# Kernel optimization log

Hardware: AMD Instinct MI355X
Metric: run time of the kernel (lower is better)

## Reference

```python
import jax, jax.numpy as jnp
import numpy as np

V, D, S, L, H, NC = 32000, 768, 1024, 4, 12, 16
HS = D // H
B = 8

def _layernorm(x, w, b, eps=1e-5):
    mu = jnp.mean(x, axis=-1, keepdims=True)
    var = jnp.mean(jnp.square(x - mu), axis=-1, keepdims=True)
    return (x - mu) * jax.lax.rsqrt(var + eps) * w + b


def setup_inputs() -> dict:
    key = jax.random.key(0)
    ks = jax.random.split(key, 24)
    s = 0.02
    inp = {
        "x": jax.random.randint(ks[0], (B, S), 0, V, dtype=jnp.int64) if jax.config.jax_enable_x64 else jax.random.randint(ks[0], (B, S), 0, V, dtype=jnp.int32),
        "attention_mask": jnp.ones((B, S), dtype=jnp.int32),
        "tok_emb": jax.random.normal(ks[1], (V, D), jnp.float32) * s,
        "pos_emb": jax.random.normal(ks[2], (S, D), jnp.float32) * s,
        "Wq": jax.random.normal(ks[3], (L, H, D, HS), jnp.float32) * s,
        "Wk": jax.random.normal(ks[4], (L, H, D, HS), jnp.float32) * s,
        "Wv": jax.random.normal(ks[5], (L, H, D, HS), jnp.float32) * s,
        "Wo": jax.random.normal(ks[6], (L, D, D), jnp.float32) * s,
        "bo": jnp.zeros((L, D), jnp.float32),
        "ln1_w": jnp.ones((L, D), jnp.float32),
        "ln1_b": jnp.zeros((L, D), jnp.float32),
        "ln2_w": jnp.ones((L, D), jnp.float32),
        "ln2_b": jnp.zeros((L, D), jnp.float32),
        "W1": jax.random.normal(ks[7], (L, D, 4 * D), jnp.float32) * s,
        "b1": jnp.zeros((L, 4 * D), jnp.float32),
        "W2": jax.random.normal(ks[8], (L, 4 * D, D), jnp.float32) * s,
        "b2": jnp.zeros((L, D), jnp.float32),
        "lnf_w": jnp.ones((D,), jnp.float32),
        "lnf_b": jnp.zeros((D,), jnp.float32),
        "cW1": jax.random.normal(ks[9], (D, 4 * D), jnp.float32) * s,
        "cb1": jnp.zeros((4 * D,), jnp.float32),
        "cW2": jax.random.normal(ks[10], (4 * D, NC), jnp.float32) * s,
        "cb2": jnp.zeros((NC,), jnp.float32),
    }
    return inp


def reference(x, attention_mask, tok_emb, pos_emb, Wq, Wk, Wv, Wo, bo,
              ln1_w, ln1_b, ln2_w, ln2_b, W1, b1, W2, b2,
              lnf_w, lnf_b, cW1, cb1, cW2, cb2):
    b, s = x.shape
    h = tok_emb[x] + pos_emb[jnp.arange(s)][None, :, :]  # [B,S,D]
    key_mask = (attention_mask == 0)[:, None, None, :]   # [B,1,1,S] masks keys
    scale = jnp.asarray(D, h.dtype) ** -0.5              # NOTE: scales by embed_dim, as in source
    for l in range(L):
        xn = _layernorm(h, ln1_w[l], ln1_b[l])
        q = jnp.einsum('bsd,hde->bhse', xn, Wq[l])
        k = jnp.einsum('bsd,hde->bhse', xn, Wk[l])
        v = jnp.einsum('bsd,hde->bhse', xn, Wv[l])
        wei = jnp.einsum('bhqe,bhke->bhqk', q, k) * scale
        wei = jnp.where(key_mask, -jnp.inf, wei)
        att = jax.nn.softmax(wei, axis=-1)               # dropout = identity (eval)
        out = jnp.einsum('bhqk,bhke->bhqe', att, v)      # [B,H,S,HS]
        out = out.transpose(0, 2, 1, 3).reshape(b, s, D)  # concat heads
        h = h + out @ Wo[l] + bo[l]
        xn2 = _layernorm(h, ln2_w[l], ln2_b[l])
        h = h + jax.nn.relu(xn2 @ W1[l] + b1[l]) @ W2[l] + b2[l]
    h = _layernorm(h, lnf_w, lnf_b)
    last = h[:, -1, :]                                   # pool=None -> last position
    logits = jax.nn.relu(last @ cW1 + cb1) @ cW2 + cb2
    return logits
```

## Files before the change

kernel.cpp:

```cpp
#include <hip/hip_runtime.h>
#include <hip/hip_bf16.h>

#define D_MODEL 768
#define SEQ     1024
#define NB      8
#define NHEAD   12
#define HS      64
#define NLAYER  4
#define DFF     3072
#define NCLS    16
#define MROWS   (NB*SEQ)

typedef float f32x4  __attribute__((ext_vector_type(4)));
typedef short bf16x8 __attribute__((ext_vector_type(8)));

__device__ __forceinline__ short f2bf_s(float x) {
    __hip_bfloat16 h = __float2bfloat16(x);
    union { __hip_bfloat16 h; short s; } u; u.h = h; return u.s;
}

__device__ __forceinline__ void gld16(const void* g, void* l) {
    __builtin_amdgcn_global_load_lds((const __attribute__((address_space(1))) void*)g,
                                     (__attribute__((address_space(3))) void*)l, 16, 0, 0);
}

__global__ __launch_bounds__(256) void embed_kernel(
    const int* __restrict__ x, const float* __restrict__ tok,
    const float* __restrict__ pos, float* __restrict__ h)
{
    int row = blockIdx.x;
    int s   = row & (SEQ - 1);
    int t   = threadIdx.x;
    int id  = x[row];
    const float* te = tok + (size_t)id * D_MODEL;
    const float* pe = pos + (size_t)s  * D_MODEL;
    float* hr = h + (size_t)row * D_MODEL;
    for (int d = t; d < D_MODEL; d += 256) hr[d] = te[d] + pe[d];
}

template<int BF16OUT>
__global__ __launch_bounds__(256) void ln_kernel(
    const float* __restrict__ in, const float* __restrict__ w,
    const float* __restrict__ b, void* __restrict__ outv,
    int row_stride, int row_offset)
{
    __shared__ float part[8];
    int r = blockIdx.x;
    const float* xr = in + (size_t)(r * row_stride + row_offset) * D_MODEL;
    int t = threadIdx.x, wave = t >> 6, lane = t & 63;
    float v0 = xr[t], v1 = xr[t + 256], v2 = xr[t + 512];
    float s = v0 + v1 + v2;
    #pragma unroll
    for (int off = 32; off; off >>= 1) s += __shfl_xor(s, off);
    if (lane == 0) part[wave] = s;
    __syncthreads();
    float mu = (part[0] + part[1] + part[2] + part[3]) * (1.f / D_MODEL);
    float d0 = v0 - mu, d1 = v1 - mu, d2 = v2 - mu;
    float q = d0*d0 + d1*d1 + d2*d2;
    #pragma unroll
    for (int off = 32; off; off >>= 1) q += __shfl_xor(q, off);
    if (lane == 0) part[4 + wave] = q;
    __syncthreads();
    float rstd = rsqrtf((part[4] + part[5] + part[6] + part[7]) * (1.f / D_MODEL) + 1e-5f);
    float y0 = d0 * rstd * w[t]       + b[t];
    float y1 = d1 * rstd * w[t + 256] + b[t + 256];
    float y2 = d2 * rstd * w[t + 512] + b[t + 512];
    if (BF16OUT) {
        __hip_bfloat16* yr = (__hip_bfloat16*)outv + (size_t)r * D_MODEL;
        yr[t] = __float2bfloat16(y0); yr[t+256] = __float2bfloat16(y1); yr[t+512] = __float2bfloat16(y2);
    } else {
        float* yr = (float*)outv + (size_t)r * D_MODEL;
        yr[t] = y0; yr[t+256] = y1; yr[t+512] = y2;
    }
}

template<int MODE>
__global__ __launch_bounds__(256) void convw_kernel(
    const float* __restrict__ W, __hip_bfloat16* __restrict__ BT,
    int K, int N, size_t in_stride, size_t out_stride)
{
    __shared__ __hip_bfloat16 sT[64][72];
    W  += (size_t)blockIdx.z * in_stride;
    BT += (size_t)blockIdx.z * out_stride;
    int k0 = blockIdx.x * 64, n0 = blockIdx.y * 64;
    int t = threadIdx.x;
    int kl = t >> 4, nl4 = (t & 15) * 4;
    #pragma unroll
    for (int i = 0; i < 4; i++) {
        int k = k0 + kl + i * 16;
        int n = n0 + nl4;
        const float* src = (MODE == 0) ? (W + (size_t)k * N + n)
                                       : (W + ((size_t)(n >> 6) * K + k) * 64 + (n & 63));
        float4 v = *(const float4*)src;
        sT[nl4 + 0][kl + i*16] = __float2bfloat16(v.x);
        sT[nl4 + 1][kl + i*16] = __float2bfloat16(v.y);
        sT[nl4 + 2][kl + i*16] = __float2bfloat16(v.z);
        sT[nl4 + 3][kl + i*16] = __float2bfloat16(v.w);
    }
    __syncthreads();
    int nl = t >> 2, seg = (t & 3) * 16;
    uint4* dst = (uint4*)(BT + (size_t)(n0 + nl) * K + k0 + seg);
    dst[0] = *(uint4*)&sT[nl][seg];
    dst[1] = *(uint4*)&sT[nl][seg + 8];
}

template<int OMODE>
__global__ __launch_bounds__(256, 3) void gemm128(
    const __hip_bfloat16* __restrict__ A, const __hip_bfloat16* __restrict__ BT,
    const float* __restrict__ bias, const float* __restrict__ res,
    void* __restrict__ Cv, int M, int N, int K, int relu)
{
    __shared__ short sA[3][128 * 32];
    __shared__ short sB[3][128 * 32];
    int t = threadIdx.x;
    int wave = t >> 6, lane = t & 63;
    int l16 = lane & 15, quad = (lane >> 4) & 3;
    int wm = wave >> 1, wn = wave & 1;
    int bm = blockIdx.x * 128, bn = blockIdx.y * 128;

    int kbeg = 0, kend = K;
    if (OMODE == 3) { int KS = K >> 1; kbeg = blockIdx.z * KS; kend = kbeg + KS; }
    int nsteps = (kend - kbeg) >> 5;

    int u = lane >> 2;
    int skey = ((u & 3) ^ ((u >> 2) & 3));
    int sseg = (lane & 3) ^ skey;
    int c0 = wave * 2, c1 = wave * 2 + 1;
    int rA0 = c0 * 16 + u, rA1 = c1 * 16 + u;
    int fkey = ((l16 & 3) ^ ((l16 >> 2) & 3));

    const f32x4 zf = {0.f, 0.f, 0.f, 0.f};
    f32x4 acc[4][4];
    #pragma unroll
    for (int mi = 0; mi < 4; mi++)
        #pragma unroll
        for (int ni = 0; ni < 4; ni++) acc[mi][ni] = zf;

    const __hip_bfloat16* pA0 = A  + (size_t)(bm + rA0) * K + kbeg + sseg * 8;
    const __hip_bfloat16* pA1 = A  + (size_t)(bm + rA1) * K + kbeg + sseg * 8;
    const __hip_bfloat16* pB0 = BT + (size_t)(bn + rA0) * K + kbeg + sseg * 8;
    const __hip_bfloat16* pB1 = BT + (size_t)(bn + rA1) * K + kbeg + sseg * 8;

    #define STAGE(bufi, kk) do { \
        gld16(pA0 + (kk), &sA[bufi][c0 * 512]); \
        gld16(pA1 + (kk), &sA[bufi][c1 * 512]); \
        gld16(pB0 + (kk), &sB[bufi][c0 * 512]); \
        gld16(pB1 + (kk), &sB[bufi][c1 * 512]); \
    } while (0)

    STAGE(0, 0);
    if (nsteps > 1) STAGE(1, 32);

    int bufr = 0, bufs = 2;
    for (int it = 0; it < nsteps; ++it) {
        if (it + 1 < nsteps) { asm volatile("s_waitcnt vmcnt(4)" ::: "memory"); }
        else                 { asm volatile("s_waitcnt vmcnt(0)" ::: "memory"); }
        __builtin_amdgcn_sched_barrier(0);
        __builtin_amdgcn_s_barrier();
        __builtin_amdgcn_sched_barrier(0);

        const short* curA = &sA[bufr][0];
        const short* curB = &sB[bufr][0];
        bf16x8 aF[4], bF[4];
        #pragma unroll
        for (int mi = 0; mi < 4; mi++)
            aF[mi] = *(const bf16x8*)&curA[(wm * 64 + mi * 16 + l16) * 32 + ((quad ^ fkey) * 8)];
        #pragma unroll
        for (int ni = 0; ni < 4; ni++)
            bF[ni] = *(const bf16x8*)&curB[(wn * 64 + ni * 16 + l16) * 32 + ((quad ^ fkey) * 8)];

        asm volatile("s_waitcnt lgkmcnt(0)" ::: "memory");
        __builtin_amdgcn_sched_barrier(0);
        __builtin_amdgcn_s_barrier();
        __builtin_amdgcn_sched_barrier(0);

        if (it + 2 < nsteps) STAGE(bufs, (it + 2) * 32);

        #pragma unroll
        for (int ni = 0; ni < 4; ni++)
            #pragma unroll
            for (int mi = 0; mi < 4; mi++)
                acc[mi][ni] = __builtin_amdgcn_mfma_f32_16x16x32_bf16(aF[mi], bF[ni], acc[mi][ni], 0, 0, 0);

        bufr = (bufr == 2) ? 0 : bufr + 1;
        bufs = (bufs == 2) ? 0 : bufs + 1;
    }
    #undef STAGE

    #pragma unroll
    for (int mi = 0; mi < 4; mi++) {
        #pragma unroll
        for (int ni = 0; ni < 4; ni++) {
            int row0 = bm + wm * 64 + mi * 16 + quad * 4;
            int col  = bn + wn * 64 + ni * 16 + l16;
            #pragma unroll
            for (int r = 0; r < 4; r++) {
                int row = row0 + r;
                float v = acc[mi][ni][r];
                if (OMODE == 3) {
                    float* C = (float*)Cv;
                    if (blockIdx.z == 0 && bias) v += bias[col];
                    unsafeAtomicAdd(&C[(size_t)row * N + col], v);
                    continue;
                }
                if (OMODE != 1 && bias) v += bias[col];
                if (relu) v = fmaxf(v, 0.f);
                if (OMODE == 0) {
                    float* C = (float*)Cv;
                    if (res) v += res[(size_t)row * N + col];
                    C[(size_t)row * N + col] = v;
                } else if (OMODE == 1) {
                    int which = col / D_MODEL, cc = col % D_MODEL;
                    int bb = row >> 10, ss = row & 1023, hh = cc >> 6, e = cc & 63;
                    ((__hip_bfloat16*)Cv)[(size_t)which * MROWS * D_MODEL +
                        (((size_t)(bb * NHEAD + hh)) * SEQ + ss) * HS + e] = __float2bfloat16(v);
                } else {
                    ((__hip_bfloat16*)Cv)[(size_t)row * N + col] = __float2bfloat16(v);
                }
            }
        }
    }
    (void)M;
}

__global__ __launch_bounds__(256) void vtrans_kernel(
    const __hip_bfloat16* __restrict__ vb, __hip_bfloat16* __restrict__ vt)
{
    __shared__ short tile[64][66];
    int bh = blockIdx.x, st = blockIdx.y;
    const short* src = (const short*)vb + ((size_t)bh * SEQ + st * 64) * HS;
    int t = threadIdx.x;
    #pragma unroll
    for (int i = 0; i < 2; i++) {
        int slot = t + i * 256;
        int row = slot >> 3, seg = slot & 7;
        *(uint4*)&tile[row][seg * 8] = *(const uint4*)(src + row * HS + seg * 8);
    }
    __syncthreads();
    short* dst = (short*)vt + (size_t)bh * HS * SEQ + st * 64;
    #pragma unroll
    for (int i = 0; i < 2; i++) {
        int slot = t + i * 256;
        int e = slot >> 3, seg = slot & 7;
        union { uint4 u; short s[8]; } pk;
        #pragma unroll
        for (int j = 0; j < 8; j++) pk.s[j] = tile[seg * 8 + j][e];
        *(uint4*)(dst + (size_t)e * SEQ + seg * 8) = pk.u;
    }
}

__global__ __launch_bounds__(128, 2) void attn_mfma_kernel(
    const __hip_bfloat16* __restrict__ q, const __hip_bfloat16* __restrict__ k,
    const __hip_bfloat16* __restrict__ v, const int* __restrict__ mask,
    __hip_bfloat16* __restrict__ ao)
{
    __shared__ short sK[2][64 * 64];
    __shared__ short sVT[2][64 * 64];
    __shared__ short sP[2][64 * 64];
    __shared__ float mskf[SEQ];
    int bid = blockIdx.x;
    int xcd = bid & 7, j = bid >> 3;
    int bh  = ((j >> 3) << 3) | xcd;
    int qt8 = j & 7;
    int b = bh / NHEAD, hh = bh % NHEAD;
    int t = threadIdx.x, w = t >> 6, lane = t & 63;
    int l16 = lane & 15, quad = lane >> 4;
    const float scale = 0.036084391824351615f;
    const f32x4 zf = {0.f, 0.f, 0.f, 0.f};

    #pragma unroll
    for (int i = 0; i < 8; i++) {
        int idx = t + i * 128;
        mskf[idx] = mask[b * SEQ + idx] ? 0.f : -1e30f;
    }

    int qb0 = qt8 * 128 + w * 64;
    const __hip_bfloat16* qbase = q + ((size_t)bh * SEQ + qb0) * HS;
    bf16x8 qf[4][2];
    #pragma unroll
    for (int qt = 0; qt < 4; qt++)
        #pragma unroll
        for (int s = 0; s < 2; s++)
            qf[qt][s] = *(const bf16x8*)(qbase + (qt * 16 + l16) * HS + s * 32 + quad * 8);

    f32x4 accO[4][4];
    float m_st[4], l_st[4];
    #pragma unroll
    for (int dt = 0; dt < 4; dt++)
        #pragma unroll
        for (int qt = 0; qt < 4; qt++) accO[dt][qt] = zf;
    #pragma unroll
    for (int qt = 0; qt < 4; qt++) { m_st[qt] = -1e30f; l_st[qt] = 0.f; }

    int rowL = lane >> 3;
    int sgl = ((lane & 7) ^ ((lane >> 3) & 7)) * 8;
    const __hip_bfloat16* kg0 = k + ((size_t)bh * SEQ) * HS;
    const __hip_bfloat16* vtg0 = v + (size_t)bh * HS * SEQ;
    short* myP = &sP[w][0];

    #pragma unroll
    for (int i = 0; i < 4; i++) {
        int c = w * 4 + i;
        int rr = c * 8 + rowL;
        gld16(kg0  + (size_t)rr * HS  + sgl, (char*)&sK[0][0]  + c * 1024);
        gld16(vtg0 + (size_t)rr * SEQ + sgl, (char*)&sVT[0][0] + c * 1024);
    }
    __syncthreads();

    int buf = 0;
    for (int kc = 0; kc < 16; kc++) {
        if (kc < 15) {
            const __hip_bfloat16* kg  = kg0  + (size_t)(kc + 1) * 64 * HS;
            const __hip_bfloat16* vtg = vtg0 + (kc + 1) * 64;
            #pragma unroll
            for (int i = 0; i < 4; i++) {
                int c = w * 4 + i;
                int rr = c * 8 + rowL;
                gld16(kg  + (size_t)rr * HS  + sgl, (char*)&sK[buf ^ 1][0]  + c * 1024);
                gld16(vtg + (size_t)rr * SEQ + sgl, (char*)&sVT[buf ^ 1][0] + c * 1024);
            }
        }
        short* cK  = &sK[buf][0];
        short* cVT = &sVT[buf][0];

        bf16x8 vf[4][2];
        #pragma unroll
        for (int dt = 0; dt < 4; dt++)
            #pragma unroll
            for (int s = 0; s < 2; s++)
                vf[dt][s] = *(bf16x8*)&cVT[(dt * 16 + l16) * 64 + (((s * 4 + quad) ^ (l16 & 7)) * 8)];
        f32x4 sc[4][4];
        #pragma unroll
        for (int kt = 0; kt < 4; kt++) {
            bf16x8 kf0 = *(bf16x8*)&cK[(kt * 16 + l16) * 64 + ((quad ^ (l16 & 7)) * 8)];
            bf16x8 kf1 = *(bf16x8*)&cK[(kt * 16 + l16) * 64 + (((4 + quad) ^ (l16 & 7)) * 8)];
            #pragma unroll
            for (int qt = 0; qt < 4; qt++) {
                f32x4 c = __builtin_amdgcn_mfma_f32_16x16x32_bf16(kf0, qf[qt][0], zf, 0, 0, 0);
                sc[kt][qt] = __builtin_amdgcn_mfma_f32_16x16x32_bf16(kf1, qf[qt][1], c, 0, 0, 0);
            }
        }
        #pragma unroll
        for (int kt = 0; kt < 4; kt++) {
            f32x4 mk = *(f32x4*)&mskf[kc * 64 + kt * 16 + quad * 4];
            #pragma unroll
            for (int qt = 0; qt < 4; qt++)
                #pragma unroll
                for (int r = 0; r < 4; r++)
                    sc[kt][qt][r] = sc[kt][qt][r] * scale + mk[r];
        }
        #pragma unroll
        for (int qt = 0; qt < 4; qt++) {
            float rm = -1e30f;
            #pragma unroll
            for (int kt = 0; kt < 4; kt++)
                #pragma unroll
                for (int r = 0; r < 4; r++) rm = fmaxf(rm, sc[kt][qt][r]);
            rm = fmaxf(rm, __shfl_xor(rm, 16));
            rm = fmaxf(rm, __shfl_xor(rm, 32));
            float mnew = fmaxf(m_st[qt], rm);
            float corr = __expf(m_st[qt] - mnew);
            m_st[qt] = mnew;
            float ps = 0.f;
            #pragma unroll
            for (int kt = 0; kt < 4; kt++) {
                union { uint2 u; short s[4]; } pk;
                #pragma unroll
                for (int r = 0; r < 4; r++) {
                    float p = __expf(sc[kt][qt][r] - mnew);
                    ps += p;
                    pk.s[r] = f2bf_s(p);
                }
                *(uint2*)&myP[(qt * 16 + l16) * 64 +
                              (((kt * 2 + (quad >> 1)) ^ (l16 & 7)) * 8) + (quad & 1) * 4] = pk.u;
            }
            ps += __shfl_xor(ps, 16);
            ps += __shfl_xor(ps, 32);
            l_st[qt] = l_st[qt] * corr + ps;
            #pragma unroll
            for (int dt = 0; dt < 4; dt++) accO[dt][qt] *= corr;
        }
        asm volatile("" ::: "memory");
        #pragma unroll
        for (int qt = 0; qt < 4; qt++) {
            bf16x8 pf0 = *(bf16x8*)&myP[(qt * 16 + l16) * 64 + ((quad ^ (l16 & 7)) * 8)];
            bf16x8 pf1 = *(bf16x8*)&myP[(qt * 16 + l16) * 64 + (((4 + quad) ^ (l16 & 7)) * 8)];
            #pragma unroll
            for (int dt = 0; dt < 4; dt++) {
                accO[dt][qt] = __builtin_amdgcn_mfma_f32_16x16x32_bf16(vf[dt][0], pf0, accO[dt][qt], 0, 0, 0);
                accO[dt][qt] = __builtin_amdgcn_mfma_f32_16x16x32_bf16(vf[dt][1], pf1, accO[dt][qt], 0, 0, 0);
            }
        }
        __syncthreads();
        buf ^= 1;
    }

    #pragma unroll
    for (int qt = 0; qt < 4; qt++) {
        float inv = 1.f / l_st[qt];
        int row = qb0 + qt * 16 + l16;
        __hip_bfloat16* orow = ao + ((size_t)(b * SEQ + row)) * D_MODEL + hh * HS;
        #pragma unroll
        for (int dt = 0; dt < 4; dt++) {
            union { uint2 u; short s[4]; } pk;
            #pragma unroll
            for (int r = 0; r < 4; r++) pk.s[r] = f2bf_s(accO[dt][qt][r] * inv);
            *(uint2*)(orow + dt * 16 + quad * 4) = pk.u;
        }
    }
}

__global__ __launch_bounds__(256) void fc1_kernel(
    const float* __restrict__ A, const float* __restrict__ W,
    const float* __restrict__ bias, float* __restrict__ out)
{
    __shared__ float sa[D_MODEL];
    int row = blockIdx.x, t = threadIdx.x;
    for (int i = t; i < D_MODEL; i += 256) sa[i] = A[(size_t)row * D_MODEL + i];
    __syncthreads();
    int col = blockIdx.y * 256 + t;
    float s = 0.f;
    #pragma unroll 8
    for (int kk = 0; kk < D_MODEL; kk++) s = fmaf(sa[kk], W[(size_t)kk * DFF + col], s);
    s += bias[col];
    out[(size_t)row * DFF + col] = fmaxf(s, 0.f);
}

__global__ __launch_bounds__(256) void fc2_kernel(
    const float* __restrict__ A, const float* __restrict__ W,
    const float* __restrict__ bias, float* __restrict__ out)
{
    __shared__ float wred[4][NCLS];
    int row = blockIdx.x, t = threadIdx.x;
    int wave = t >> 6, lane = t & 63;
    const float* a = A + (size_t)row * DFF;
    float acc[NCLS];
    #pragma unroll
    for (int c = 0; c < NCLS; c++) acc[c] = 0.f;
    for (int kk = t; kk < DFF; kk += 256) {
        float av = a[kk];
        const float4* wr = (const float4*)(W + (size_t)kk * NCLS);
        float4 w0 = wr[0], w1 = wr[1], w2 = wr[2], w3 = wr[3];
        acc[0]  = fmaf(av, w0.x, acc[0]);  acc[1]  = fmaf(av, w0.y, acc[1]);
        acc[2]  = fmaf(av, w0.z, acc[2]);  acc[3]  = fmaf(av, w0.w, acc[3]);
        acc[4]  = fmaf(av, w1.x, acc[4]);  acc[5]  = fmaf(av, w1.y, acc[5]);
        acc[6]  = fmaf(av, w1.z, acc[6]);  acc[7]  = fmaf(av, w1.w, acc[7]);
        acc[8]  = fmaf(av, w2.x, acc[8]);  acc[9]  = fmaf(av, w2.y, acc[9]);
        acc[10] = fmaf(av, w2.z, acc[10]); acc[11] = fmaf(av, w2.w, acc[11]);
        acc[12] = fmaf(av, w3.x, acc[12]); acc[13] = fmaf(av, w3.y, acc[13]);
        acc[14] = fmaf(av, w3.z, acc[14]); acc[15] = fmaf(av, w3.w, acc[15]);
    }
    #pragma unroll
    for (int c = 0; c < NCLS; c++)
        #pragma unroll
        for (int off = 32; off; off >>= 1) acc[c] += __shfl_down(acc[c], off);
    if (lane == 0)
        #pragma unroll
        for (int c = 0; c < NCLS; c++) wred[wave][c] = acc[c];
    __syncthreads();
    if (t < NCLS)
        out[row * NCLS + t] = wred[0][t] + wred[1][t] + wred[2][t] + wred[3][t] + bias[t];
}

extern "C" void kernel_launch(void* const* d_in, const int* in_sizes, int n_in,
                              void* d_out, int out_size, void* d_ws, size_t ws_size,
                              hipStream_t stream)
{
    const int*   x     = (const int*)  d_in[0];
    const int*   amask = (const int*)  d_in[1];
    const float* tok   = (const float*)d_in[2];
    const float* pos   = (const float*)d_in[3];
    const float* Wq    = (const float*)d_in[4];
    const float* Wk    = (const float*)d_in[5];
    const float* Wv    = (const float*)d_in[6];
    const float* Wo    = (const float*)d_in[7];
    const float* bo    = (const float*)d_in[8];
    const float* ln1w  = (const float*)d_in[9];
    const float* ln1b  = (const float*)d_in[10];
    const float* ln2w  = (const float*)d_in[11];
    const float* ln2b  = (const float*)d_in[12];
    const float* W1    = (const float*)d_in[13];
    const float* b1    = (const float*)d_in[14];
    const float* W2    = (const float*)d_in[15];
    const float* b2    = (const float*)d_in[16];
    const float* lnfw  = (const float*)d_in[17];
    const float* lnfb  = (const float*)d_in[18];
    const float* cW1   = (const float*)d_in[19];
    const float* cb1   = (const float*)d_in[20];
    const float* cW2   = (const float*)d_in[21];
    const float* cb2   = (const float*)d_in[22];

    char* base = (char*)d_ws;
    const size_t MD = (size_t)MROWS * D_MODEL;
    float* h = (float*)base;                         base += MD * 4;
    __hip_bfloat16* xn = (__hip_bfloat16*)base;      base += MD * 2;
    __hip_bfloat16* qb = (__hip_bfloat16*)base;      base += MD * 2;
    __hip_bfloat16* kb = (__hip_bfloat16*)base;      base += MD * 2;
    __hip_bfloat16* vb = (__hip_bfloat16*)base;      base += MD * 2;
    __hip_bfloat16* vT = (__hip_bfloat16*)base;      base += MD * 2;
    __hip_bfloat16* ff = (__hip_bfloat16*)base;      base += (size_t)MROWS * DFF * 2;
    float* lnf = (float*)base;                       base += (size_t)NB * D_MODEL * 4;
    float* cls = (float*)base;                       base += (size_t)NB * DFF * 4;
    __hip_bfloat16* wQKV = (__hip_bfloat16*)base;    base += (size_t)NLAYER * 3 * D_MODEL * D_MODEL * 2;
    __hip_bfloat16* wTo = (__hip_bfloat16*)base;     base += (size_t)NLAYER * D_MODEL * D_MODEL * 2;
    __hip_bfloat16* wT1 = (__hip_bfloat16*)base;     base += (size_t)NLAYER * D_MODEL * DFF * 2;
    __hip_bfloat16* wT2 = (__hip_bfloat16*)base;     base += (size_t)NLAYER * DFF * D_MODEL * 2;

    const size_t SQW = (size_t)D_MODEL * D_MODEL;
    const size_t SFF = (size_t)D_MODEL * DFF;

    convw_kernel<1><<<dim3(12,12,4), 256, 0, stream>>>(Wq, wQKV + 0 * SQW, D_MODEL, D_MODEL, SQW, 3 * SQW);
    convw_kernel<1><<<dim3(12,12,4), 256, 0, stream>>>(Wk, wQKV + 1 * SQW, D_MODEL, D_MODEL, SQW, 3 * SQW);
    convw_kernel<1><<<dim3(12,12,4), 256, 0, stream>>>(Wv, wQKV + 2 * SQW, D_MODEL, D_MODEL, SQW, 3 * SQW);
    convw_kernel<0><<<dim3(12,12,4), 256, 0, stream>>>(Wo, wTo, D_MODEL, D_MODEL, SQW, SQW);
    convw_kernel<0><<<dim3(12,48,4), 256, 0, stream>>>(W1, wT1, D_MODEL, DFF, SFF, SFF);
    convw_kernel<0><<<dim3(48,12,4), 256, 0, stream>>>(W2, wT2, DFF, D_MODEL, SFF, SFF);

    embed_kernel<<<MROWS, 256, 0, stream>>>(x, tok, pos, h);

    dim3 gQKV(MROWS / 128, (3 * D_MODEL) / 128);
    dim3 gDS(MROWS / 128, D_MODEL / 128, 2);
    dim3 gF(MROWS / 128, DFF / 128);
    for (int l = 0; l < NLAYER; l++) {
        ln_kernel<1><<<MROWS, 256, 0, stream>>>(h, ln1w + l * D_MODEL, ln1b + l * D_MODEL, xn, 1, 0);
        gemm128<1><<<gQKV, 256, 0, stream>>>(xn, wQKV + l * 3 * SQW, nullptr, nullptr, qb, MROWS, 3 * D_MODEL, D_MODEL, 0);
        vtrans_kernel<<<dim3(NB * NHEAD, SEQ / 64), 256, 0, stream>>>(vb, vT);
        attn_mfma_kernel<<<NB * NHEAD * 8, 128, 0, stream>>>(qb, kb, vT, amask, xn);
        gemm128<3><<<gDS, 256, 0, stream>>>(xn, wTo + l * SQW, bo + l * D_MODEL, nullptr, h, MROWS, D_MODEL, D_MODEL, 0);
        ln_kernel<1><<<MROWS, 256, 0, stream>>>(h, ln2w + l * D_MODEL, ln2b + l * D_MODEL, xn, 1, 0);
        gemm128<2><<<gF, 256, 0, stream>>>(xn, wT1 + l * SFF, b1 + l * DFF, nullptr, ff, MROWS, DFF, D_MODEL, 1);
        gemm128<3><<<gDS, 256, 0, stream>>>(ff, wT2 + l * SFF, b2 + l * D_MODEL, nullptr, h, MROWS, D_MODEL, DFF, 0);
    }
    ln_kernel<0><<<NB, 256, 0, stream>>>(h, lnfw, lnfb, lnf, SEQ, SEQ - 1);
    fc1_kernel<<<dim3(NB, DFF / 256), 256, 0, stream>>>(lnf, cW1, cb1, cls);
    fc2_kernel<<<NB, 256, 0, stream>>>(cls, cW2, cb2, (float*)d_out);
}
```

Measured before the change: 1.675 ms.

## Add 256x256 bf16 MFMA GEMM kernel for QKV and FFN projections

Result: slower. 1.930 ms (+15.2%).

```diff
diff --git a/kernel.cpp b/kernel.cpp
--- a/kernel.cpp
+++ b/kernel.cpp
@@ -102,6 +102,134 @@
     uint4* dst = (uint4*)(BT + (size_t)(n0 + nl) * K + k0 + seg);
     dst[0] = *(uint4*)&sT[nl][seg];
     dst[1] = *(uint4*)&sT[nl][seg + 8];
+}
+
+template<int OMODE>
+__global__ __launch_bounds__(512, 1) void gemm256(
+    const __hip_bfloat16* __restrict__ A, const __hip_bfloat16* __restrict__ BT,
+    const float* __restrict__ bias, const float* __restrict__ res,
+    void* __restrict__ Cv, int M, int N, int K, int relu)
+{
+    __shared__ short sA[2][256 * 64];
+    __shared__ short sB[2][256 * 64];
+    int t = threadIdx.x;
+    int wave = t >> 6, lane = t & 63;
+    int l16 = lane & 15, quad = (lane >> 4) & 3;
+    int wm = wave >> 2, wn = wave & 3;
+    int bm = blockIdx.x * 256, bn = blockIdx.y * 256;
+
+    int kbeg = 0, kend = K;
+    if (OMODE == 3) { int KS = K >> 1; kbeg = blockIdx.z * KS; kend = kbeg + KS; }
+    int nt = (kend - kbeg) >> 6;
+
+    int rowL = lane >> 3;
+    int sgl = ((lane & 7) ^ ((lane >> 3) & 7)) * 8;
+
+    const f32x4 zf = {0.f, 0.f, 0.f, 0.f};
+    f32x4 acc[8][4];
+    #pragma unroll
+    for (int mi = 0; mi < 8; mi++)
+        #pragma unroll
+        for (int ni = 0; ni < 4; ni++) acc[mi][ni] = zf;
+
+    #define STAGE256(d, kk) do { \
+        _Pragma("unroll") \
+        for (int i = 0; i < 4; i++) { \
+            int c = i * 8 + wave; \
+            gld16(A  + (size_t)(bm + c * 8 + rowL) * K + (kk) + sgl, &sA[d][c * 512]); \
+            gld16(BT + (size_t)(bn + c * 8 + rowL) * K + (kk) + sgl, &sB[d][c * 512]); \
+        } \
+    } while (0)
+
+    #define LDA256(d, mi, kk) \
+        (*(const bf16x8*)&sA[d][((wm << 7) + (mi) * 16 + l16) * 64 + ((((kk) * 4 + quad) ^ (l16 & 7)) * 8)])
+    #define LDB256(d, ni, kk) \
+        (*(const bf16x8*)&sB[d][((wn << 6) + (ni) * 16 + l16) * 64 + ((((kk) * 4 + quad) ^ (l16 & 7)) * 8)])
+
+    #define MFMA_PAIR(m0) do { \
+        _Pragma("unroll") \
+        for (int mi = (m0); mi < (m0) + 2; mi++) \
+            _Pragma("unroll") \
+            for (int ni = 0; ni < 4; ni++) \
+                _Pragma("unroll") \
+                for (int kk = 0; kk < 2; kk++) \
+                    acc[mi][ni] = __builtin_amdgcn_mfma_f32_16x16x32_bf16(aF[mi][kk], bF[ni][kk], acc[mi][ni], 0, 0, 0); \
+    } while (0)
+
+    STAGE256(0, kbeg);
+
+    #pragma unroll 1
+    for (int t2 = 0; t2 < nt; ++t2) {
+        int d = t2 & 1;
+        asm volatile("s_waitcnt vmcnt(0)" ::: "memory");
+        __builtin_amdgcn_sched_barrier(0);
+        __builtin_amdgcn_s_barrier();
+        __builtin_amdgcn_sched_barrier(0);
+
+        bf16x8 bF[4][2], aF[8][2];
+        #pragma unroll
+        for (int ni = 0; ni < 4; ni++)
+            #pragma unroll
+            for (int kk = 0; kk < 2; kk++) bF[ni][kk] = LDB256(d, ni, kk);
+        #pragma unroll
+        for (int kk = 0; kk < 2; kk++) { aF[0][kk] = LDA256(d, 0, kk); aF[1][kk] = LDA256(d, 1, kk); }
+
+        if (t2 + 1 < nt) STAGE256(d ^ 1, kbeg + (t2 + 1) * 64);
+
+        #pragma unroll
+        for (int kk = 0; kk < 2; kk++) { aF[2][kk] = LDA256(d, 2, kk); aF[3][kk] = LDA256(d, 3, kk); }
+        asm volatile("s_waitcnt lgkmcnt(4)" ::: "memory");
+        __builtin_amdgcn_sched_barrier(0);
+        __builtin_amdgcn_s_setprio(1); MFMA_PAIR(0); __builtin_amdgcn_s_setprio(0);
+        #pragma unroll
+        for (int kk = 0; kk < 2; kk++) { aF[4][kk] = LDA256(d, 4, kk); aF[5][kk] = LDA256(d, 5, kk); }
+        asm volatile("s_waitcnt lgkmcnt(4)" ::: "memory");
+        __builtin_amdgcn_sched_barrier(0);
+        __builtin_amdgcn_s_setprio(1); MFMA_PAIR(2); __builtin_amdgcn_s_setprio(0);
+        #pragma unroll
+        for (int kk = 0; kk < 2; kk++) { aF[6][kk] = LDA256(d, 6, kk); aF[7][kk] = LDA256(d, 7, kk); }
+        asm volatile("s_waitcnt lgkmcnt(4)" ::: "memory");
+        __builtin_amdgcn_sched_barrier(0);
+        __builtin_amdgcn_s_setprio(1); MFMA_PAIR(4); __builtin_amdgcn_s_setprio(0);
+        asm volatile("s_waitcnt lgkmcnt(0)" ::: "memory");
+        __builtin_amdgcn_sched_barrier(0);
+        __builtin_amdgcn_s_setprio(1); MFMA_PAIR(6); __builtin_amdgcn_s_setprio(0);
+    }
+    #undef STAGE256
+    #undef LDA256
+    #undef LDB256
+    #undef MFMA_PAIR
+
+    #pragma unroll
+    for (int mi = 0; mi < 8; mi++) {
+        #pragma unroll
+        for (int ni = 0; ni < 4; ni++) {
+            int row0 = bm + wm * 128 + mi * 16 + quad * 4;
+            int col  = bn + wn * 64 + ni * 16 + l16;
+            #pragma unroll
+            for (int r = 0; r < 4; r++) {
+                int row = row0 + r;
+                float v = acc[mi][ni][r];
+                if (OMODE == 3) {
+                    float* C = (float*)Cv;
+                    if (blockIdx.z == 0 && bias) v += bias[col];
+                    unsafeAtomicAdd(&C[(size_t)row * N + col], v);
+                    continue;
+                }
+                if (bias) v += bias[col];
+                if (relu) v = fmaxf(v, 0.f);
+                if (OMODE == 1) {
+                    int which = col / D_MODEL, cc = col % D_MODEL;
+                    int bb = row >> 10, ss = row & 1023, hh = cc >> 6, e = cc & 63;
+                    ((__hip_bfloat16*)Cv)[(size_t)which * MROWS * D_MODEL +
+                        (((size_t)(bb * NHEAD + hh)) * SEQ + ss) * HS + e] = __float2bfloat16(v);
+                } else {
+                    ((__hip_bfloat16*)Cv)[(size_t)row * N + col] = __float2bfloat16(v);
+                }
+            }
+        }
+    }
+    (void)M; (void)res;
 }
 
 template<int OMODE>
@@ -518,18 +646,19 @@
 
     embed_kernel<<<MROWS, 256, 0, stream>>>(x, tok, pos, h);
 
-    dim3 gQKV(MROWS / 128, (3 * D_MODEL) / 128);
+    dim3 gQKV(MROWS / 256, (3 * D_MODEL) / 256);
+    dim3 gF1(MROWS / 256, DFF / 256);
+    dim3 gF2(MROWS / 256, D_MODEL / 256, 2);
     dim3 gDS(MROWS / 128, D_MODEL / 128, 2);
-    dim3 gF(MROWS / 128, DFF / 128);
     for (int l = 0; l < NLAYER; l++) {
         ln_kernel<1><<<MROWS, 256, 0, stream>>>(h, ln1w + l * D_MODEL, ln1b + l * D_MODEL, xn, 1, 0);
-        gemm128<1><<<gQKV, 256, 0, stream>>>(xn, wQKV + l * 3 * SQW, nullptr, nullptr, qb, MROWS, 3 * D_MODEL, D_MODEL, 0);
+        gemm256<1><<<gQKV, 512, 0, stream>>>(xn, wQKV + l * 3 * SQW, nullptr, nullptr, qb, MROWS, 3 * D_MODEL, D_MODEL, 0);
         vtrans_kernel<<<dim3(NB * NHEAD, SEQ / 64), 256, 0, stream>>>(vb, vT);
         attn_mfma_kernel<<<NB * NHEAD * 8, 128, 0, stream>>>(qb, kb, vT, amask, xn);
         gemm128<3><<<gDS, 256, 0, stream>>>(xn, wTo + l * SQW, bo + l * D_MODEL, nullptr, h, MROWS, D_MODEL, D_MODEL, 0);
         ln_kernel<1><<<MROWS, 256, 0, stream>>>(h, ln2w + l * D_MODEL, ln2b + l * D_MODEL, xn, 1, 0);
-        gemm128<2><<<gF, 256, 0, stream>>>(xn, wT1 + l * SFF, b1 + l * DFF, nullptr, ff, MROWS, DFF, D_MODEL, 1);
-        gemm128<3><<<gDS, 256, 0, stream>>>(ff, wT2 + l * SFF, b2 + l * D_MODEL, nullptr, h, MROWS, D_MODEL, DFF, 0);
+        gemm256<2><<<gF1, 512, 0, stream>>>(xn, wT1 + l * SFF, b1 + l * DFF, nullptr, ff, MROWS, DFF, D_MODEL, 1);
+        gemm256<3><<<gF2, 512, 0, stream>>>(ff, wT2 + l * SFF, b2 + l * D_MODEL, nullptr, h, MROWS, D_MODEL, DFF, 0);
     }
     ln_kernel<0><<<NB, 256, 0, stream>>>(h, lnfw, lnfb, lnf, SEQ, SEQ - 1);
     fc1_kernel<<<dim3(NB, DFF / 256), 256, 0, stream>>>(lnf, cW1, cb1, cls);
```

## Fuse V transpose into QKV GEMM epilogue and widen attention blocks to four waves

Applied to the files above, without the earlier changes.

Result: faster. 1.629 ms (-2.7%).

```diff
diff --git a/kernel.cpp b/kernel.cpp
--- a/kernel.cpp
+++ b/kernel.cpp
@@ -193,6 +193,23 @@
         for (int ni = 0; ni < 4; ni++) {
             int row0 = bm + wm * 64 + mi * 16 + quad * 4;
             int col  = bn + wn * 64 + ni * 16 + l16;
+            if (OMODE == 1) {
+                int which = col / D_MODEL, cc = col % D_MODEL;
+                int hh = cc >> 6, e = cc & 63;
+                int bb = row0 >> 10, ss0 = row0 & 1023;
+                union { uint2 u; short s[4]; } pk;
+                #pragma unroll
+                for (int r = 0; r < 4; r++) pk.s[r] = f2bf_s(acc[mi][ni][r]);
+                __hip_bfloat16* dstb = (__hip_bfloat16*)Cv + (size_t)which * MROWS * D_MODEL;
+                if (which == 2) {
+                    *(uint2*)(dstb + ((size_t)(bb * NHEAD + hh)) * HS * SEQ + (size_t)e * SEQ + ss0) = pk.u;
+                } else {
+                    short* p = (short*)(dstb + (((size_t)(bb * NHEAD + hh)) * SEQ + ss0) * HS + e);
+                    #pragma unroll
+                    for (int r = 0; r < 4; r++) p[r * HS] = pk.s[r];
+                }
+                continue;
+            }
             #pragma unroll
             for (int r = 0; r < 4; r++) {
                 int row = row0 + r;
@@ -203,17 +220,12 @@
                     unsafeAtomicAdd(&C[(size_t)row * N + col], v);
                     continue;
                 }
-                if (OMODE != 1 && bias) v += bias[col];
+                if (bias) v += bias[col];
                 if (relu) v = fmaxf(v, 0.f);
                 if (OMODE == 0) {
                     float* C = (float*)Cv;
                     if (res) v += res[(size_t)row * N + col];
                     C[(size_t)row * N + col] = v;
-                } else if (OMODE == 1) {
-                    int which = col / D_MODEL, cc = col % D_MODEL;
-                    int bb = row >> 10, ss = row & 1023, hh = cc >> 6, e = cc & 63;
-                    ((__hip_bfloat16*)Cv)[(size_t)which * MROWS * D_MODEL +
-                        (((size_t)(bb * NHEAD + hh)) * SEQ + ss) * HS + e] = __float2bfloat16(v);
                 } else {
                     ((__hip_bfloat16*)Cv)[(size_t)row * N + col] = __float2bfloat16(v);
                 }
@@ -223,45 +235,19 @@
     (void)M;
 }
 
-__global__ __launch_bounds__(256) void vtrans_kernel(
-    const __hip_bfloat16* __restrict__ vb, __hip_bfloat16* __restrict__ vt)
-{
-    __shared__ short tile[64][66];
-    int bh = blockIdx.x, st = blockIdx.y;
-    const short* src = (const short*)vb + ((size_t)bh * SEQ + st * 64) * HS;
-    int t = threadIdx.x;
-    #pragma unroll
-    for (int i = 0; i < 2; i++) {
-        int slot = t + i * 256;
-        int row = slot >> 3, seg = slot & 7;
-        *(uint4*)&tile[row][seg * 8] = *(const uint4*)(src + row * HS + seg * 8);
-    }
-    __syncthreads();
-    short* dst = (short*)vt + (size_t)bh * HS * SEQ + st * 64;
-    #pragma unroll
-    for (int i = 0; i < 2; i++) {
-        int slot = t + i * 256;
-        int e = slot >> 3, seg = slot & 7;
-        union { uint4 u; short s[8]; } pk;
-        #pragma unroll
-        for (int j = 0; j < 8; j++) pk.s[j] = tile[seg * 8 + j][e];
-        *(uint4*)(dst + (size_t)e * SEQ + seg * 8) = pk.u;
-    }
-}
-
-__global__ __launch_bounds__(128, 2) void attn_mfma_kernel(
+__global__ __launch_bounds__(256, 2) void attn_mfma_kernel(
     const __hip_bfloat16* __restrict__ q, const __hip_bfloat16* __restrict__ k,
     const __hip_bfloat16* __restrict__ v, const int* __restrict__ mask,
     __hip_bfloat16* __restrict__ ao)
 {
     __shared__ short sK[2][64 * 64];
     __shared__ short sVT[2][64 * 64];
-    __shared__ short sP[2][64 * 64];
+    __shared__ short sP[4][64 * 64];
     __shared__ float mskf[SEQ];
     int bid = blockIdx.x;
     int xcd = bid & 7, j = bid >> 3;
-    int bh  = ((j >> 3) << 3) | xcd;
-    int qt8 = j & 7;
+    int bh  = ((j >> 2) << 3) | xcd;
+    int qt4 = j & 3;
     int b = bh / NHEAD, hh = bh % NHEAD;
     int t = threadIdx.x, w = t >> 6, lane = t & 63;
     int l16 = lane & 15, quad = lane >> 4;
@@ -269,12 +255,12 @@
     const f32x4 zf = {0.f, 0.f, 0.f, 0.f};
 
     #pragma unroll
-    for (int i = 0; i < 8; i++) {
-        int idx = t + i * 128;
+    for (int i = 0; i < 4; i++) {
+        int idx = t + i * 256;
         mskf[idx] = mask[b * SEQ + idx] ? 0.f : -1e30f;
     }
 
-    int qb0 = qt8 * 128 + w * 64;
+    int qb0 = qt4 * 256 + w * 64;
     const __hip_bfloat16* qbase = q + ((size_t)bh * SEQ + qb0) * HS;
     bf16x8 qf[4][2];
     #pragma unroll
@@ -299,8 +285,8 @@
     short* myP = &sP[w][0];
 
     #pragma unroll
-    for (int i = 0; i < 4; i++) {
-        int c = w * 4 + i;
+    for (int i = 0; i < 2; i++) {
+        int c = w * 2 + i;
         int rr = c * 8 + rowL;
         gld16(kg0  + (size_t)rr * HS  + sgl, (char*)&sK[0][0]  + c * 1024);
         gld16(vtg0 + (size_t)rr * SEQ + sgl, (char*)&sVT[0][0] + c * 1024);
@@ -313,8 +299,8 @@
             const __hip_bfloat16* kg  = kg0  + (size_t)(kc + 1) * 64 * HS;
             const __hip_bfloat16* vtg = vtg0 + (kc + 1) * 64;
             #pragma unroll
-            for (int i = 0; i < 4; i++) {
-                int c = w * 4 + i;
+            for (int i = 0; i < 2; i++) {
+                int c = w * 2 + i;
                 int rr = c * 8 + rowL;
                 gld16(kg  + (size_t)rr * HS  + sgl, (char*)&sK[buf ^ 1][0]  + c * 1024);
                 gld16(vtg + (size_t)rr * SEQ + sgl, (char*)&sVT[buf ^ 1][0] + c * 1024);
@@ -505,6 +491,7 @@
     __hip_bfloat16* wTo = (__hip_bfloat16*)base;     base += (size_t)NLAYER * D_MODEL * D_MODEL * 2;
     __hip_bfloat16* wT1 = (__hip_bfloat16*)base;     base += (size_t)NLAYER * D_MODEL * DFF * 2;
     __hip_bfloat16* wT2 = (__hip_bfloat16*)base;     base += (size_t)NLAYER * DFF * D_MODEL * 2;
+    (void)vT;
 
     const size_t SQW = (size_t)D_MODEL * D_MODEL;
     const size_t SFF = (size_t)D_MODEL * DFF;
@@ -524,8 +511,7 @@
     for (int l = 0; l < NLAYER; l++) {
         ln_kernel<1><<<MROWS, 256, 0, stream>>>(h, ln1w + l * D_MODEL, ln1b + l * D_MODEL, xn, 1, 0);
         gemm128<1><<<gQKV, 256, 0, stream>>>(xn, wQKV + l * 3 * SQW, nullptr, nullptr, qb, MROWS, 3 * D_MODEL, D_MODEL, 0);
-        vtrans_kernel<<<dim3(NB * NHEAD, SEQ / 64), 256, 0, stream>>>(vb, vT);
-        attn_mfma_kernel<<<NB * NHEAD * 8, 128, 0, stream>>>(qb, kb, vT, amask, xn);
+        attn_mfma_kernel<<<NB * NHEAD * 4, 256, 0, stream>>>(qb, kb, vb, amask, xn);
         gemm128<3><<<gDS, 256, 0, stream>>>(xn, wTo + l * SQW, bo + l * D_MODEL, nullptr, h, MROWS, D_MODEL, D_MODEL, 0);
         ln_kernel<1><<<MROWS, 256, 0, stream>>>(h, ln2w + l * D_MODEL, ln2b + l * D_MODEL, xn, 1, 0);
         gemm128<2><<<gF, 256, 0, stream>>>(xn, wT1 + l * SFF, b1 + l * DFF, nullptr, ff, MROWS, DFF, D_MODEL, 1);
```
